# Performance work log

Measured on AMD Instinct MI355X. Metric: run time of the kernel, lower is better.

The kernel has to match this reference:

```python
import jax, jax.numpy as jnp
import numpy as np

N = 50000
E = 800000
IN_DIM, HID, OUT = 128, 64, 64
SLOPE = 0.2  # PyG GATConv default negative_slope


def gat_conv(x, W, a_src, a_dst, b, src, dst):
    """Single-head PyG GATConv, add_self_loops=False."""
    h = x @ W                                  # [N, F]
    alpha_s = h @ a_src                        # [N]
    alpha_d = h @ a_dst                        # [N]
    e = jax.nn.leaky_relu(alpha_s[src] + alpha_d[dst], SLOPE)   # [E]
    # segment softmax over incoming edges of each destination node
    m = jax.ops.segment_max(e, dst, num_segments=N)             # [N]
    w = jnp.exp(e - m[dst])                                     # [E]
    z = jax.ops.segment_sum(w, dst, num_segments=N)             # [N]
    alpha = w / z[dst]                                          # [E]
    out = jax.ops.segment_sum(h[src] * alpha[:, None], dst, num_segments=N)
    return out + b


def setup_inputs() -> dict:
    key = jax.random.key(0)
    ks = jax.random.split(key, 12)
    x = jax.random.normal(ks[0], (N, IN_DIM), dtype=jnp.float32)
    edge_index = jax.random.randint(ks[1], (2, E), 0, N, dtype=jnp.int64)
    s1 = 1.0 / np.sqrt(IN_DIM)
    s2 = 1.0 / np.sqrt(HID)
    return {
        "x": x,
        "edge_index": edge_index,
        "W1": jax.random.normal(ks[2], (IN_DIM, HID), dtype=jnp.float32) * s1,
        "att_src1": jax.random.normal(ks[3], (HID,), dtype=jnp.float32) * s2,
        "att_dst1": jax.random.normal(ks[4], (HID,), dtype=jnp.float32) * s2,
        "b1": jnp.zeros((HID,), dtype=jnp.float32),
        "W2": jax.random.normal(ks[5], (HID, OUT), dtype=jnp.float32) * s2,
        "att_src2": jax.random.normal(ks[6], (OUT,), dtype=jnp.float32) / np.sqrt(OUT),
        "att_dst2": jax.random.normal(ks[7], (OUT,), dtype=jnp.float32) / np.sqrt(OUT),
        "b2": jnp.zeros((OUT,), dtype=jnp.float32),
    }


def reference(x, edge_index, W1, att_src1, att_dst1, b1, W2, att_src2, att_dst2, b2):
    src, dst = edge_index[0], edge_index[1]
    h = gat_conv(x, W1, att_src1, att_dst1, b1, src, dst)
    h = jax.nn.relu(h)
    # dropout is identity in eval mode
    h = gat_conv(h, W2, att_src2, att_dst2, b2, src, dst)
    # F.normalize(p=2, dim=-1): divide by max(norm, eps)
    norm = jnp.linalg.norm(h, axis=-1, keepdims=True)
    return h / jnp.maximum(norm, 1e-12)
```

## Files before the change

kernel.cpp:

```cpp
#include <hip/hip_runtime.h>
#include <hip/hip_fp16.h>
#include <math.h>

#define NNODES 50000
#define NEDGES 800000
#define NBUCK 256
#define EPB 4096
#define NBLK1 ((NEDGES + EPB - 1) / EPB)
#define SCANL (NBUCK * NBLK1)
#define SCANB ((SCANL + 1023) / 1024)
#define FCAP 8192


__global__ __launch_bounds__(256) void k_bcount(const int* __restrict__ dst,
                                                int* __restrict__ bcnt) {
    __shared__ int h[NBUCK];
    int t = threadIdx.x, b = blockIdx.x;
    h[t] = 0;
    __syncthreads();
    int beg = b * EPB, end = min(beg + EPB, NEDGES);
    for (int e = beg + t; e < end; e += 256) atomicAdd(&h[dst[e] >> 8], 1);
    __syncthreads();
    bcnt[t * NBLK1 + b] = h[t];
}

__global__ void k_scan_block(const int* __restrict__ in, int* __restrict__ out,
                             int* __restrict__ partial, int n) {
    __shared__ int tmp[1024];
    int t = threadIdx.x;
    int i = blockIdx.x * 1024 + t;
    int v = (i < n) ? in[i] : 0;
    tmp[t] = v;
    __syncthreads();
    for (int off = 1; off < 1024; off <<= 1) {
        int u = (t >= off) ? tmp[t - off] : 0;
        __syncthreads();
        tmp[t] += u;
        __syncthreads();
    }
    if (i < n) out[i] = tmp[t] - v;
    if (t == 1023) partial[blockIdx.x] = tmp[t];
}

__device__ __forceinline__ void scan_partials(const int* __restrict__ partial, int* sp) {
    int t = threadIdx.x;
    if (t < 64) {
        int v = (t < SCANB) ? partial[t] : 0;
        int incl = v;
        #pragma unroll
        for (int off = 1; off < 64; off <<= 1) {
            int u = __shfl_up(incl, off, 64);
            if (t >= off) incl += u;
        }
        if (t < SCANB) sp[t] = incl - v;
    }
    __syncthreads();
}

__global__ __launch_bounds__(256) void k_bscatter(const int* __restrict__ src,
                                                  const int* __restrict__ dst,
                                                  const int* __restrict__ boffs,
                                                  const int* __restrict__ partial,
                                                  int* __restrict__ ep) {
    __shared__ int cur[NBUCK];
    __shared__ int sp[SCANB];
    int t = threadIdx.x, b = blockIdx.x;
    scan_partials(partial, sp);
    int idx = t * NBLK1 + b;
    cur[t] = boffs[idx] + sp[idx >> 10];
    __syncthreads();
    int beg = b * EPB, end = min(beg + EPB, NEDGES);
    for (int e = beg + t; e < end; e += 256) {
        int d = dst[e];
        int pos = atomicAdd(&cur[d >> 8], 1);
        ep[pos] = (src[e] << 8) | (d & 255);
    }
}

__global__ __launch_bounds__(512) void k_fine(const int* __restrict__ ep,
                                              const int* __restrict__ boffs,
                                              const int* __restrict__ partial,
                                              int* __restrict__ offs,
                                              int* __restrict__ esrc) {
    __shared__ int h[NBUCK];
    __shared__ int cur[NBUCK];
    __shared__ int sp[SCANB];
    __shared__ int stg[FCAP];
    __shared__ int srt[FCAP];
    int t = threadIdx.x, buck = blockIdx.x;
    scan_partials(partial, sp);
    int bi = buck * NBLK1;
    int base = boffs[bi] + sp[bi >> 10];
    int endp;
    if (buck == NBUCK - 1) endp = NEDGES;
    else {
        int ei2 = (buck + 1) * NBLK1;
        endp = boffs[ei2] + sp[ei2 >> 10];
    }
    int cnt = endp - base;
    bool fits = (cnt <= FCAP);

    if (t < NBUCK) h[t] = 0;
    __syncthreads();
    if (fits) {
        for (int j = t; j < cnt; j += 512) stg[j] = ep[base + j];
        __syncthreads();
        for (int j = t; j < cnt; j += 512) atomicAdd(&h[stg[j] & 255], 1);
    } else {
        for (int i = base + t; i < endp; i += 512) atomicAdd(&h[ep[i] & 255], 1);
    }
    __syncthreads();
    int v = (t < NBUCK) ? h[t] : 0;
    for (int off = 1; off < 256; off <<= 1) {
        int u = (t >= off && t < NBUCK) ? h[t - off] : 0;
        __syncthreads();
        if (t < NBUCK) h[t] += u;
        __syncthreads();
    }
    if (t < NBUCK) {
        int excl = h[t] - v;
        int node = buck * 256 + t;
        if (node <= NNODES) offs[node] = base + excl;
        cur[t] = excl;
    }
    __syncthreads();
    if (fits) {
        for (int j = t; j < cnt; j += 512) {
            int p = stg[j];
            int pos = atomicAdd(&cur[p & 255], 1);
            srt[pos] = p >> 8;
        }
        __syncthreads();
        for (int j = t; j < cnt; j += 512) esrc[base + j] = srt[j];
    } else {
        for (int i = base + t; i < endp; i += 512) {
            int p = ep[i];
            int pos = atomicAdd(&cur[p & 255], 1);
            esrc[base + pos] = p >> 8;
        }
    }
}


__device__ __forceinline__ void fma4(float4& a, float s, const float4& w) {
    a.x = fmaf(s, w.x, a.x);
    a.y = fmaf(s, w.y, a.y);
    a.z = fmaf(s, w.z, a.z);
    a.w = fmaf(s, w.w, a.w);
}

template<int K, int XH>
__global__ __launch_bounds__(256, 2) void k_gemm_att(
    const void* __restrict__ Xv, const float* __restrict__ W,
    const float* __restrict__ a_src, const float* __restrict__ a_dst,
    __half* __restrict__ H, float* __restrict__ AS, float* __restrict__ AD, int N)
{
    constexpr int KF = K / 4;
    constexpr int KFS = (K == 128) ? 5 : 4;
    __shared__ float Xs[64 * K];
    __shared__ float Ws[K * 64];
    int t = threadIdx.x;
    int n0 = blockIdx.x * 64;

    const float4* W4 = (const float4*)W;
    #pragma unroll
    for (int f = t; f < K * 16; f += 256)
        ((float4*)Ws)[f] = W4[f];
    #pragma unroll
    for (int f = t; f < 64 * KF; f += 256) {
        int r = f >> KFS, k4 = f & (KF - 1);
        float4 v = {0.f, 0.f, 0.f, 0.f};
        if (n0 + r < N) {
            if (XH) {
                union { uint2 u; __half2 h2[2]; } c;
                c.u = ((const uint2*)Xv)[(size_t)(n0 + r) * KF + k4];
                float2 lo = __half22float2(c.h2[0]);
                float2 hi = __half22float2(c.h2[1]);
                v = make_float4(lo.x, lo.y, hi.x, hi.y);
            } else {
                v = ((const float4*)Xv)[(size_t)(n0 + r) * KF + k4];
            }
        }
        ((float4*)&Xs[r * K])[k4 ^ ((r >> 2) & 3)] = v;
    }
    __syncthreads();

    int tr = t >> 4, tc = t & 15;
    int xi = tr & 3;
    const float4* xr0 = (const float4*)&Xs[(tr * 4 + 0) * K];
    const float4* xr1 = (const float4*)&Xs[(tr * 4 + 1) * K];
    const float4* xr2 = (const float4*)&Xs[(tr * 4 + 2) * K];
    const float4* xr3 = (const float4*)&Xs[(tr * 4 + 3) * K];
    float4 acc0 = {}, acc1 = {}, acc2 = {}, acc3 = {};

    #pragma unroll 2
    for (int k4 = 0; k4 < KF; ++k4) {
        int sl = k4 ^ xi;
        float4 x0 = xr0[sl], x1 = xr1[sl], x2 = xr2[sl], x3 = xr3[sl];
        float4 w0 = *(const float4*)&Ws[(k4 * 4 + 0) * 64 + tc * 4];
        float4 w1 = *(const float4*)&Ws[(k4 * 4 + 1) * 64 + tc * 4];
        float4 w2 = *(const float4*)&Ws[(k4 * 4 + 2) * 64 + tc * 4];
        float4 w3 = *(const float4*)&Ws[(k4 * 4 + 3) * 64 + tc * 4];
        fma4(acc0, x0.x, w0); fma4(acc0, x0.y, w1); fma4(acc0, x0.z, w2); fma4(acc0, x0.w, w3);
        fma4(acc1, x1.x, w0); fma4(acc1, x1.y, w1); fma4(acc1, x1.z, w2); fma4(acc1, x1.w, w3);
        fma4(acc2, x2.x, w0); fma4(acc2, x2.y, w1); fma4(acc2, x2.z, w2); fma4(acc2, x2.w, w3);
        fma4(acc3, x3.x, w0); fma4(acc3, x3.y, w1); fma4(acc3, x3.z, w2); fma4(acc3, x3.w, w3);
    }

    float4 asv = *(const float4*)&a_src[tc * 4];
    float4 adv = *(const float4*)&a_dst[tc * 4];
    float4 accs[4] = {acc0, acc1, acc2, acc3};
    #pragma unroll
    for (int i = 0; i < 4; ++i) {
        int row = n0 + tr * 4 + i;
        if (row < N) {
            float4 a = accs[i];
            float s1 = a.x * asv.x + a.y * asv.y + a.z * asv.z + a.w * asv.w;
            float s2 = a.x * adv.x + a.y * adv.y + a.z * adv.z + a.w * adv.w;
            #pragma unroll
            for (int o = 1; o < 16; o <<= 1) {
                s1 += __shfl_xor(s1, o, 64);
                s2 += __shfl_xor(s2, o, 64);
            }
            union { __half2 h2[2]; uint2 u; } pk;
            pk.h2[0] = __floats2half2_rn(a.x, a.y);
            pk.h2[1] = __floats2half2_rn(a.z, a.w);
            *(uint2*)&H[(size_t)row * 64 + tc * 4] = pk.u;
            if (tc == 0) { AS[row] = s1; AD[row] = s2; }
        }
    }
}

template<int RELU, int NORM, int OUTH>
__global__ __launch_bounds__(256) void k_agg(
    const int* __restrict__ esrc, const int* __restrict__ offs,
    const __half* __restrict__ H, const float* __restrict__ AS,
    const float* __restrict__ AD, const float* __restrict__ bias,
    void* __restrict__ outv, int N)
{
    __shared__ int2 sm[4][64];
    int gid = blockIdx.x * blockDim.x + threadIdx.x;
    int w = gid >> 6;
    int lane = gid & 63;
    int wid = threadIdx.x >> 6;
    int n0 = 2 * w;
    if (n0 >= N) return;
    int half = lane >> 5, fp = lane & 31;
    int nh = n0 + half;
    bool valid = nh < N;
    int beg = valid ? offs[nh] : 0;
    int end = valid ? offs[nh + 1] : 0;
    int deg = end - beg;
    int degO = __shfl_xor(deg, 32, 64);
    int dm = max(deg, degO);
    float2 bp = ((const float2*)bias)[fp];

    if (dm <= 32) {
        float add = valid ? AD[nh] : 0.f;
        int s = 0;
        float logit = -3.0e38f;
        if (fp < deg) {
            s = esrc[beg + fp];
            float l0 = AS[s] + add;
            logit = (l0 > 0.f) ? l0 : 0.2f * l0;
        }
        float m = logit;
        #pragma unroll
        for (int o = 16; o > 0; o >>= 1) m = fmaxf(m, __shfl_xor(m, o, 64));
        float wg = (fp < deg) ? __expf(logit - m) : 0.f;
        float z = wg;
        #pragma unroll
        for (int o = 16; o > 0; o >>= 1) z += __shfl_xor(z, o, 64);
        sm[wid][lane] = make_int2(s, __float_as_int(wg));

        const __half2* H2 = (const __half2*)H;
        float2 a0 = {0.f, 0.f}, a1 = {0.f, 0.f};
        int base = half * 32;
        int k = 0;
        for (; k + 1 < dm; k += 2) {
            int4 v = *(const int4*)&sm[wid][base + k];
            float2 h0 = __half22float2(H2[(size_t)v.x * 32 + fp]);
            float2 h1 = __half22float2(H2[(size_t)v.z * 32 + fp]);
            float w0 = __int_as_float(v.y), w1 = __int_as_float(v.w);
            a0.x = fmaf(w0, h0.x, a0.x); a0.y = fmaf(w0, h0.y, a0.y);
            a1.x = fmaf(w1, h1.x, a1.x); a1.y = fmaf(w1, h1.y, a1.y);
        }
        if (k < dm) {
            int2 v = sm[wid][base + k];
            float2 h0 = __half22float2(H2[(size_t)v.x * 32 + fp]);
            float w0 = __int_as_float(v.y);
            a0.x = fmaf(w0, h0.x, a0.x); a0.y = fmaf(w0, h0.y, a0.y);
        }
        float2 acc = {a0.x + a1.x, a0.y + a1.y};
        float rz = (deg > 0) ? (1.0f / z) : 0.f;
        float2 val2 = make_float2(fmaf(acc.x, rz, bp.x), fmaf(acc.y, rz, bp.y));
        if (RELU) { val2.x = fmaxf(val2.x, 0.f); val2.y = fmaxf(val2.y, 0.f); }
        if (NORM) {
            float ss = val2.x * val2.x + val2.y * val2.y;
            #pragma unroll
            for (int o = 16; o > 0; o >>= 1) ss += __shfl_xor(ss, o, 64);
            float inv = 1.0f / fmaxf(sqrtf(ss), 1e-12f);
            val2.x *= inv; val2.y *= inv;
        }
        if (valid) {
            if (OUTH) ((__half2*)outv)[(size_t)nh * 32 + fp] = __floats2half2_rn(val2.x, val2.y);
            else      ((float2*)outv)[(size_t)nh * 32 + fp] = val2;
        }
        return;
    }

    #pragma unroll 1
    for (int side = 0; side < 2; ++side) {
        int n = n0 + side;
        if (n >= N) break;
        int b2 = offs[n], e2 = offs[n + 1];
        int dg = e2 - b2;
        float add = AD[n];
        if (dg <= 64) {
            int s = 0;
            float logit = -3.0e38f;
            if (lane < dg) {
                s = esrc[b2 + lane];
                float l0 = AS[s] + add;
                logit = (l0 > 0.f) ? l0 : 0.2f * l0;
            }
            float m = logit;
            #pragma unroll
            for (int o = 32; o > 0; o >>= 1) m = fmaxf(m, __shfl_xor(m, o, 64));
            float wg = (lane < dg) ? __expf(logit - m) : 0.f;
            float z = wg;
            #pragma unroll
            for (int o = 32; o > 0; o >>= 1) z += __shfl_xor(z, o, 64);
            sm[wid][lane] = make_int2(s, __float_as_int(wg));
            const __half2* H2 = (const __half2*)H;
            float2 a0 = {0.f, 0.f};
            for (int k = half; k < dg; k += 2) {
                int2 v = sm[wid][k];
                float2 h0 = __half22float2(H2[(size_t)v.x * 32 + fp]);
                float w0 = __int_as_float(v.y);
                a0.x = fmaf(w0, h0.x, a0.x); a0.y = fmaf(w0, h0.y, a0.y);
            }
            a0.x += __shfl_xor(a0.x, 32, 64);
            a0.y += __shfl_xor(a0.y, 32, 64);
            float rz = (dg > 0) ? (1.0f / z) : 0.f;
            float2 val2 = make_float2(fmaf(a0.x, rz, bp.x), fmaf(a0.y, rz, bp.y));
            if (RELU) { val2.x = fmaxf(val2.x, 0.f); val2.y = fmaxf(val2.y, 0.f); }
            if (NORM) {
                float ss = val2.x * val2.x + val2.y * val2.y;
                #pragma unroll
                for (int o = 16; o > 0; o >>= 1) ss += __shfl_xor(ss, o, 64);
                float inv = 1.0f / fmaxf(sqrtf(ss), 1e-12f);
                val2.x *= inv; val2.y *= inv;
            }
            if (half == 0) {
                if (OUTH) ((__half2*)outv)[(size_t)n * 32 + fp] = __floats2half2_rn(val2.x, val2.y);
                else      ((float2*)outv)[(size_t)n * 32 + fp] = val2;
            }
        } else {
            float m = -3.0e38f, z = 0.f, acc = 0.f;
            for (int i = b2; i < e2; ++i) {
                int s = esrc[i];
                float l0 = AS[s] + add;
                l0 = (l0 > 0.f) ? l0 : 0.2f * l0;
                float mn = fmaxf(m, l0);
                float sc = __expf(m - mn);
                float wgt = __expf(l0 - mn);
                z = z * sc + wgt;
                acc = acc * sc + wgt * __half2float(H[(size_t)s * 64 + lane]);
                m = mn;
            }
            float val = acc / z + bias[lane];
            if (RELU) val = fmaxf(val, 0.f);
            if (NORM) {
                float ss = val * val;
                #pragma unroll
                for (int o = 32; o > 0; o >>= 1) ss += __shfl_xor(ss, o, 64);
                val = val / fmaxf(sqrtf(ss), 1e-12f);
            }
            if (OUTH) ((__half*)outv)[(size_t)n * 64 + lane] = __float2half(val);
            else      ((float*)outv)[(size_t)n * 64 + lane] = val;
        }
    }
}


extern "C" void kernel_launch(void* const* d_in, const int* in_sizes, int n_in,
                              void* d_out, int out_size, void* d_ws, size_t ws_size,
                              hipStream_t stream) {
    const float* x   = (const float*)d_in[0];
    const int*   ei  = (const int*)d_in[1];
    const float* W1  = (const float*)d_in[2];
    const float* as1 = (const float*)d_in[3];
    const float* ad1 = (const float*)d_in[4];
    const float* b1  = (const float*)d_in[5];
    const float* W2  = (const float*)d_in[6];
    const float* as2 = (const float*)d_in[7];
    const float* ad2 = (const float*)d_in[8];
    const float* b2  = (const float*)d_in[9];
    const int* src = ei;
    const int* dst = ei + NEDGES;

    char* ws = (char*)d_ws;
    size_t off = 0;
    auto alloc = [&](size_t bytes) -> void* {
        void* p = ws + off;
        off = (off + bytes + 255) & ~(size_t)255;
        return p;
    };
    __half* H    = (__half*)alloc((size_t)NNODES * 64 * 2);
    __half* OUT1 = (__half*)alloc((size_t)NNODES * 64 * 2);
    float* AS    = (float*)alloc((size_t)NNODES * 4);
    float* AD    = (float*)alloc((size_t)NNODES * 4);
    int*   offs  = (int*)alloc((size_t)(NNODES + 1) * 4);
    int*   ep    = (int*)alloc((size_t)NEDGES * 4);
    int*   esrc  = (int*)alloc((size_t)NEDGES * 4);
    int*   bcnt  = (int*)alloc((size_t)SCANL * 4);
    int*   boffs = (int*)alloc((size_t)SCANL * 4);
    int*   part1 = (int*)alloc((size_t)SCANB * 4);

    k_bcount<<<NBLK1, 256, 0, stream>>>(dst, bcnt);
    k_scan_block<<<SCANB, 1024, 0, stream>>>(bcnt, boffs, part1, SCANL);
    k_bscatter<<<NBLK1, 256, 0, stream>>>(src, dst, boffs, part1, ep);
    k_fine<<<NBUCK, 512, 0, stream>>>(ep, boffs, part1, offs, esrc);

    int aggBlocks = (NNODES / 2 + 3) / 4;
    k_gemm_att<128, 0><<<(NNODES + 63) / 64, 256, 0, stream>>>(x, W1, as1, ad1, H, AS, AD, NNODES);
    k_agg<1, 0, 1><<<aggBlocks, 256, 0, stream>>>(esrc, offs, H, AS, AD, b1, OUT1, NNODES);

    k_gemm_att<64, 1><<<(NNODES + 63) / 64, 256, 0, stream>>>(OUT1, W2, as2, ad2, H, AS, AD, NNODES);
    k_agg<0, 1, 0><<<aggBlocks, 256, 0, stream>>>(esrc, offs, H, AS, AD, b2, d_out, NNODES);
}
```

Before: 118.2 us.

## Fuse layer-1 GEMM with bucket scatter kernel and vectorize bucket counting

Merges the first-layer GEMM/attention-score kernel and the edge bucket-scatter kernel into one launch, with block ranges split by blockIdx and the scatter reusing the GEMM's shared memory. This removes a kernel launch and lets independent work overlap on the GPU. EPB is doubled to halve the number of histogram/scatter blocks, bucket counting now loads dst as int4, and the second GEMM requests 3 waves per SIMD via launch bounds. The fused kernel reserves 64KB of shared memory for scatter blocks, which may limit their occupancy. The int4 load assumes dst is 16-byte aligned and that the edge count divides by 4.

```diff
diff --git a/kernel.cpp b/kernel.cpp
--- a/kernel.cpp
+++ b/kernel.cpp
@@ -5,11 +5,12 @@
 #define NNODES 50000
 #define NEDGES 800000
 #define NBUCK 256
-#define EPB 4096
+#define EPB 8192
 #define NBLK1 ((NEDGES + EPB - 1) / EPB)
 #define SCANL (NBUCK * NBLK1)
 #define SCANB ((SCANL + 1023) / 1024)
 #define FCAP 8192
+#define NGEMM1 ((NNODES + 63) / 64)
 
 
 __global__ __launch_bounds__(256) void k_bcount(const int* __restrict__ dst,
@@ -18,8 +19,15 @@
     int t = threadIdx.x, b = blockIdx.x;
     h[t] = 0;
     __syncthreads();
-    int beg = b * EPB, end = min(beg + EPB, NEDGES);
-    for (int e = beg + t; e < end; e += 256) atomicAdd(&h[dst[e] >> 8], 1);
+    const int4* d4 = (const int4*)dst;
+    int beg = b * (EPB / 4), end = min(beg + EPB / 4, NEDGES / 4);
+    for (int e = beg + t; e < end; e += 256) {
+        int4 v = d4[e];
+        atomicAdd(&h[v.x >> 8], 1);
+        atomicAdd(&h[v.y >> 8], 1);
+        atomicAdd(&h[v.z >> 8], 1);
+        atomicAdd(&h[v.w >> 8], 1);
+    }
     __syncthreads();
     bcnt[t * NBLK1 + b] = h[t];
 }
@@ -57,14 +65,124 @@
     __syncthreads();
 }
 
-__global__ __launch_bounds__(256) void k_bscatter(const int* __restrict__ src,
-                                                  const int* __restrict__ dst,
-                                                  const int* __restrict__ boffs,
-                                                  const int* __restrict__ partial,
-                                                  int* __restrict__ ep) {
-    __shared__ int cur[NBUCK];
-    __shared__ int sp[SCANB];
-    int t = threadIdx.x, b = blockIdx.x;
+
+__device__ __forceinline__ void fma4(float4& a, float s, const float4& w) {
+    a.x = fmaf(s, w.x, a.x);
+    a.y = fmaf(s, w.y, a.y);
+    a.z = fmaf(s, w.z, a.z);
+    a.w = fmaf(s, w.w, a.w);
+}
+
+template<int K, int XH>
+__device__ __forceinline__ void gemm_body(
+    float* __restrict__ Xs, float* __restrict__ Ws, int bid,
+    const void* __restrict__ Xv, const float* __restrict__ W,
+    const float* __restrict__ a_src, const float* __restrict__ a_dst,
+    __half* __restrict__ H, float* __restrict__ AS, float* __restrict__ AD, int N)
+{
+    constexpr int KF = K / 4;
+    constexpr int KFS = (K == 128) ? 5 : 4;
+    int t = threadIdx.x;
+    int n0 = bid * 64;
+
+    const float4* W4 = (const float4*)W;
+    #pragma unroll
+    for (int f = t; f < K * 16; f += 256)
+        ((float4*)Ws)[f] = W4[f];
+    #pragma unroll
+    for (int f = t; f < 64 * KF; f += 256) {
+        int r = f >> KFS, k4 = f & (KF - 1);
+        float4 v = {0.f, 0.f, 0.f, 0.f};
+        if (n0 + r < N) {
+            if (XH) {
+                union { uint2 u; __half2 h2[2]; } c;
+                c.u = ((const uint2*)Xv)[(size_t)(n0 + r) * KF + k4];
+                float2 lo = __half22float2(c.h2[0]);
+                float2 hi = __half22float2(c.h2[1]);
+                v = make_float4(lo.x, lo.y, hi.x, hi.y);
+            } else {
+                v = ((const float4*)Xv)[(size_t)(n0 + r) * KF + k4];
+            }
+        }
+        ((float4*)&Xs[r * K])[k4 ^ ((r >> 2) & 3)] = v;
+    }
+    __syncthreads();
+
+    int tr = t >> 4, tc = t & 15;
+    int xi = tr & 3;
+    const float4* xr0 = (const float4*)&Xs[(tr * 4 + 0) * K];
+    const float4* xr1 = (const float4*)&Xs[(tr * 4 + 1) * K];
+    const float4* xr2 = (const float4*)&Xs[(tr * 4 + 2) * K];
+    const float4* xr3 = (const float4*)&Xs[(tr * 4 + 3) * K];
+    float4 acc0 = {}, acc1 = {}, acc2 = {}, acc3 = {};
+
+    #pragma unroll 2
+    for (int k4 = 0; k4 < KF; ++k4) {
+        int sl = k4 ^ xi;
+        float4 x0 = xr0[sl], x1 = xr1[sl], x2 = xr2[sl], x3 = xr3[sl];
+        float4 w0 = *(const float4*)&Ws[(k4 * 4 + 0) * 64 + tc * 4];
+        float4 w1 = *(const float4*)&Ws[(k4 * 4 + 1) * 64 + tc * 4];
+        float4 w2 = *(const float4*)&Ws[(k4 * 4 + 2) * 64 + tc * 4];
+        float4 w3 = *(const float4*)&Ws[(k4 * 4 + 3) * 64 + tc * 4];
+        fma4(acc0, x0.x, w0); fma4(acc0, x0.y, w1); fma4(acc0, x0.z, w2); fma4(acc0, x0.w, w3);
+        fma4(acc1, x1.x, w0); fma4(acc1, x1.y, w1); fma4(acc1, x1.z, w2); fma4(acc1, x1.w, w3);
+        fma4(acc2, x2.x, w0); fma4(acc2, x2.y, w1); fma4(acc2, x2.z, w2); fma4(acc2, x2.w, w3);
+        fma4(acc3, x3.x, w0); fma4(acc3, x3.y, w1); fma4(acc3, x3.z, w2); fma4(acc3, x3.w, w3);
+    }
+
+    float4 asv = *(const float4*)&a_src[tc * 4];
+    float4 adv = *(const float4*)&a_dst[tc * 4];
+    float4 accs[4] = {acc0, acc1, acc2, acc3};
+    #pragma unroll
+    for (int i = 0; i < 4; ++i) {
+        int row = n0 + tr * 4 + i;
+        if (row < N) {
+            float4 a = accs[i];
+            float s1 = a.x * asv.x + a.y * asv.y + a.z * asv.z + a.w * asv.w;
+            float s2 = a.x * adv.x + a.y * adv.y + a.z * adv.z + a.w * adv.w;
+            #pragma unroll
+            for (int o = 1; o < 16; o <<= 1) {
+                s1 += __shfl_xor(s1, o, 64);
+                s2 += __shfl_xor(s2, o, 64);
+            }
+            union { __half2 h2[2]; uint2 u; } pk;
+            pk.h2[0] = __floats2half2_rn(a.x, a.y);
+            pk.h2[1] = __floats2half2_rn(a.z, a.w);
+            *(uint2*)&H[(size_t)row * 64 + tc * 4] = pk.u;
+            if (tc == 0) { AS[row] = s1; AD[row] = s2; }
+        }
+    }
+}
+
+template<int K, int XH, int MINW>
+__global__ __launch_bounds__(256, MINW) void k_gemm_att(
+    const void* __restrict__ Xv, const float* __restrict__ W,
+    const float* __restrict__ a_src, const float* __restrict__ a_dst,
+    __half* __restrict__ H, float* __restrict__ AS, float* __restrict__ AD, int N)
+{
+    __shared__ float Xs[64 * K];
+    __shared__ float Ws[K * 64];
+    gemm_body<K, XH>(Xs, Ws, blockIdx.x, Xv, W, a_src, a_dst, H, AS, AD, N);
+}
+
+
+__global__ __launch_bounds__(256, 2) void k_gemm1_bscatter(
+    const float* __restrict__ X, const float* __restrict__ W1,
+    const float* __restrict__ as1, const float* __restrict__ ad1,
+    __half* __restrict__ H, float* __restrict__ AS, float* __restrict__ AD,
+    const int* __restrict__ src, const int* __restrict__ dst,
+    const int* __restrict__ boffs, const int* __restrict__ partial,
+    int* __restrict__ ep)
+{
+    __shared__ float Xs[64 * 128];
+    __shared__ float Ws[128 * 64];
+    if (blockIdx.x < NGEMM1) {
+        gemm_body<128, 0>(Xs, Ws, blockIdx.x, X, W1, as1, ad1, H, AS, AD, NNODES);
+        return;
+    }
+    int* cur = (int*)Xs;
+    int* sp  = (int*)Ws;
+    int t = threadIdx.x, b = blockIdx.x - NGEMM1;
     scan_partials(partial, sp);
     int idx = t * NBLK1 + b;
     cur[t] = boffs[idx] + sp[idx >> 10];
@@ -137,96 +255,6 @@
             int p = ep[i];
             int pos = atomicAdd(&cur[p & 255], 1);
             esrc[base + pos] = p >> 8;
-        }
-    }
-}
-
-
-__device__ __forceinline__ void fma4(float4& a, float s, const float4& w) {
-    a.x = fmaf(s, w.x, a.x);
-    a.y = fmaf(s, w.y, a.y);
-    a.z = fmaf(s, w.z, a.z);
-    a.w = fmaf(s, w.w, a.w);
-}
-
-template<int K, int XH>
-__global__ __launch_bounds__(256, 2) void k_gemm_att(
-    const void* __restrict__ Xv, const float* __restrict__ W,
-    const float* __restrict__ a_src, const float* __restrict__ a_dst,
-    __half* __restrict__ H, float* __restrict__ AS, float* __restrict__ AD, int N)
-{
-    constexpr int KF = K / 4;
-    constexpr int KFS = (K == 128) ? 5 : 4;
-    __shared__ float Xs[64 * K];
-    __shared__ float Ws[K * 64];
-    int t = threadIdx.x;
-    int n0 = blockIdx.x * 64;
-
-    const float4* W4 = (const float4*)W;
-    #pragma unroll
-    for (int f = t; f < K * 16; f += 256)
-        ((float4*)Ws)[f] = W4[f];
-    #pragma unroll
-    for (int f = t; f < 64 * KF; f += 256) {
-        int r = f >> KFS, k4 = f & (KF - 1);
-        float4 v = {0.f, 0.f, 0.f, 0.f};
-        if (n0 + r < N) {
-            if (XH) {
-                union { uint2 u; __half2 h2[2]; } c;
-                c.u = ((const uint2*)Xv)[(size_t)(n0 + r) * KF + k4];
-                float2 lo = __half22float2(c.h2[0]);
-                float2 hi = __half22float2(c.h2[1]);
-                v = make_float4(lo.x, lo.y, hi.x, hi.y);
-            } else {
-                v = ((const float4*)Xv)[(size_t)(n0 + r) * KF + k4];
-            }
-        }
-        ((float4*)&Xs[r * K])[k4 ^ ((r >> 2) & 3)] = v;
-    }
-    __syncthreads();
-
-    int tr = t >> 4, tc = t & 15;
-    int xi = tr & 3;
-    const float4* xr0 = (const float4*)&Xs[(tr * 4 + 0) * K];
-    const float4* xr1 = (const float4*)&Xs[(tr * 4 + 1) * K];
-    const float4* xr2 = (const float4*)&Xs[(tr * 4 + 2) * K];
-    const float4* xr3 = (const float4*)&Xs[(tr * 4 + 3) * K];
-    float4 acc0 = {}, acc1 = {}, acc2 = {}, acc3 = {};
-
-    #pragma unroll 2
-    for (int k4 = 0; k4 < KF; ++k4) {
-        int sl = k4 ^ xi;
-        float4 x0 = xr0[sl], x1 = xr1[sl], x2 = xr2[sl], x3 = xr3[sl];
-        float4 w0 = *(const float4*)&Ws[(k4 * 4 + 0) * 64 + tc * 4];
-        float4 w1 = *(const float4*)&Ws[(k4 * 4 + 1) * 64 + tc * 4];
-        float4 w2 = *(const float4*)&Ws[(k4 * 4 + 2) * 64 + tc * 4];
-        float4 w3 = *(const float4*)&Ws[(k4 * 4 + 3) * 64 + tc * 4];
-        fma4(acc0, x0.x, w0); fma4(acc0, x0.y, w1); fma4(acc0, x0.z, w2); fma4(acc0, x0.w, w3);
-        fma4(acc1, x1.x, w0); fma4(acc1, x1.y, w1); fma4(acc1, x1.z, w2); fma4(acc1, x1.w, w3);
-        fma4(acc2, x2.x, w0); fma4(acc2, x2.y, w1); fma4(acc2, x2.z, w2); fma4(acc2, x2.w, w3);
-        fma4(acc3, x3.x, w0); fma4(acc3, x3.y, w1); fma4(acc3, x3.z, w2); fma4(acc3, x3.w, w3);
-    }
-
-    float4 asv = *(const float4*)&a_src[tc * 4];
-    float4 adv = *(const float4*)&a_dst[tc * 4];
-    float4 accs[4] = {acc0, acc1, acc2, acc3};
-    #pragma unroll
-    for (int i = 0; i < 4; ++i) {
-        int row = n0 + tr * 4 + i;
-        if (row < N) {
-            float4 a = accs[i];
-            float s1 = a.x * asv.x + a.y * asv.y + a.z * asv.z + a.w * asv.w;
-            float s2 = a.x * adv.x + a.y * adv.y + a.z * adv.z + a.w * adv.w;
-            #pragma unroll
-            for (int o = 1; o < 16; o <<= 1) {
-                s1 += __shfl_xor(s1, o, 64);
-                s2 += __shfl_xor(s2, o, 64);
-            }
-            union { __half2 h2[2]; uint2 u; } pk;
-            pk.h2[0] = __floats2half2_rn(a.x, a.y);
-            pk.h2[1] = __floats2half2_rn(a.z, a.w);
-            *(uint2*)&H[(size_t)row * 64 + tc * 4] = pk.u;
-            if (tc == 0) { AS[row] = s1; AD[row] = s2; }
         }
     }
 }
@@ -420,13 +448,13 @@
 
     k_bcount<<<NBLK1, 256, 0, stream>>>(dst, bcnt);
     k_scan_block<<<SCANB, 1024, 0, stream>>>(bcnt, boffs, part1, SCANL);
-    k_bscatter<<<NBLK1, 256, 0, stream>>>(src, dst, boffs, part1, ep);
+    k_gemm1_bscatter<<<NGEMM1 + NBLK1, 256, 0, stream>>>(
+        x, W1, as1, ad1, H, AS, AD, src, dst, boffs, part1, ep);
     k_fine<<<NBUCK, 512, 0, stream>>>(ep, boffs, part1, offs, esrc);
 
     int aggBlocks = (NNODES / 2 + 3) / 4;
-    k_gemm_att<128, 0><<<(NNODES + 63) / 64, 256, 0, stream>>>(x, W1, as1, ad1, H, AS, AD, NNODES);
     k_agg<1, 0, 1><<<aggBlocks, 256, 0, stream>>>(esrc, offs, H, AS, AD, b1, OUT1, NNODES);
 
-    k_gemm_att<64, 1><<<(NNODES + 63) / 64, 256, 0, stream>>>(OUT1, W2, as2, ad2, H, AS, AD, NNODES);
+    k_gemm_att<64, 1, 3><<<(NNODES + 63) / 64, 256, 0, stream>>>(OUT1, W2, as2, ad2, H, AS, AD, NNODES);
     k_agg<0, 1, 0><<<aggBlocks, 256, 0, stream>>>(esrc, offs, H, AS, AD, b2, d_out, NNODES);
 }
```

Result: no change. 117.0 us (-1.0%).
